# Performance work log

Measured on AMD Instinct MI355X. Metric: run time of the kernel, lower is better.

Reference implementation:

```python
import jax, jax.numpy as jnp
import numpy as np

B, N, D = 131072, 5, 12   # batch, objects per scene, per-object feature dim
E = 64                    # goal embedding / F1 output dim
H = E // 2                # F1 hidden dim = 32


def setup_inputs() -> dict:
    key = jax.random.key(0)
    ks = jax.random.split(key, 6)
    return {
        "obs": jax.random.normal(ks[0], (B, N, D), dtype=jnp.float32),
        "ghat": jax.random.normal(ks[1], (B, E), dtype=jnp.float32),
        "W1": jax.random.normal(ks[2], (2 * D, H), dtype=jnp.float32) * 0.1,
        "b1": jax.random.normal(ks[3], (H,), dtype=jnp.float32) * 0.1,
        "W2": jax.random.normal(ks[4], (H, E), dtype=jnp.float32) * 0.1,
        "b2": jax.random.normal(ks[5], (E,), dtype=jnp.float32) * 0.1,
    }


def reference(obs, ghat, W1, b1, W2, b2):
    b, n, d = obs.shape
    # all-pairs concat: pairs[i,j,k] = cat(obs[i,j], obs[i,k])  -> [B,N,N,2D]
    o_j = jnp.broadcast_to(obs[:, :, None, :], (b, n, n, d))
    o_k = jnp.broadcast_to(obs[:, None, :, :], (b, n, n, d))
    pairs = jnp.concatenate([o_j, o_k], axis=-1)
    # F1 MLP: Linear -> ReLU -> Linear  -> Z [B,N,N,E]
    Z = jnp.maximum(pairs @ W1 + b1, 0.0) @ W2 + b2
    # attention logits w[i,j,k] = <Z[i,j,k], ghat[i]>; softmax over all N*N pairs
    w = jnp.einsum('bjke,be->bjk', Z, ghat)
    p = jax.nn.softmax(w.reshape(b, -1), axis=1).reshape(b, n, n)
    # z_vector[i,j,k] = sum_e p[i,j,k]*Z[i,j,k,e]; zhat[i,j] = sum_k z_vector
    zhat = jnp.einsum('bjk,bjk->bj', p, Z.sum(axis=-1))  # [B,N]
    # state_rep[i,j] = cat(obs[i,j], ghat[i], zhat[i])  -> [B,N,D+E+N]
    state = jnp.concatenate([
        obs,
        jnp.broadcast_to(ghat[:, None, :], (b, n, E)),
        jnp.broadcast_to(zhat[:, None, :], (b, n, n)),
    ], axis=-1)
    return state.reshape(b, -1)  # Flatten -> [B, N*(D+E+N)] = [B, 405]
```

## Files before the change

kernel.cpp:

```cpp
#include <hip/hip_runtime.h>

#define BLOCK 256
#define NB 5
#define DD 12
#define EE 64
#define HH 32
#define ROW 81
#define OUTW 405
#define TILE 64

__global__ __launch_bounds__(BLOCK) void zhat_kernel(
    const float* __restrict__ obs, const float* __restrict__ ghat,
    const float* __restrict__ W1, const float* __restrict__ b1,
    const float* __restrict__ W2, const float* __restrict__ b2,
    float* __restrict__ zbuf, int zstride, int zoff, int B)
{
    __shared__ float s_w2s[HH];
    __shared__ float s_sb2;
    __shared__ float s_g2[BLOCK * 33];

    const int tid = threadIdx.x;

    if (tid < HH) {
        float s = 0.f;
        #pragma unroll
        for (int e = 0; e < EE; ++e) s += W2[tid * EE + e];
        s_w2s[tid] = s;
    } else if (tid == HH) {
        float s = 0.f;
        #pragma unroll
        for (int e = 0; e < EE; ++e) s += b2[e];
        s_sb2 = s;
    }

    const int i = blockIdx.x * BLOCK + tid;

    float g2[HH];
    #pragma unroll
    for (int h = 0; h < HH; ++h) g2[h] = 0.f;
    if (i < B) {
        const float* grow = ghat + (size_t)i * EE;
        #pragma unroll
        for (int e0 = 0; e0 < EE; e0 += 16) {
            float gc[16];
            const float4* gp = reinterpret_cast<const float4*>(grow + e0);
            #pragma unroll
            for (int q = 0; q < 4; ++q) {
                float4 v = gp[q];
                gc[4*q+0] = v.x; gc[4*q+1] = v.y; gc[4*q+2] = v.z; gc[4*q+3] = v.w;
            }
            #pragma unroll
            for (int h = 0; h < HH; ++h) {
                #pragma unroll
                for (int q = 0; q < 16; ++q)
                    g2[h] += W2[h * EE + e0 + q] * gc[q];
            }
        }
    }
    #pragma unroll
    for (int h = 0; h < HH; ++h) s_g2[tid * 33 + h] = g2[h];
    __syncthreads();

    if (i < B) {
        float o[NB * DD];
        {
            const float4* p = reinterpret_cast<const float4*>(obs + (size_t)i * (NB * DD));
            #pragma unroll
            for (int q = 0; q < NB * DD / 4; ++q) {
                float4 v = p[q];
                o[4*q+0] = v.x; o[4*q+1] = v.y; o[4*q+2] = v.z; o[4*q+3] = v.w;
            }
        }

        float w[NB * NB];
        float hw[NB * NB];
        #pragma unroll
        for (int q = 0; q < NB * NB; ++q) { w[q] = 0.f; hw[q] = 0.f; }

        for (int c = 0; c < HH / 8; ++c) {
            float g2c[8], w2c[8];
            #pragma unroll
            for (int hp = 0; hp < 8; ++hp) {
                g2c[hp] = s_g2[tid * 33 + c * 8 + hp];
                w2c[hp] = s_w2s[c * 8 + hp];
            }
            #pragma unroll
            for (int hp = 0; hp < 8; ++hp) {
                const int h = c * 8 + hp;
                float a[NB], bb[NB];
                #pragma unroll
                for (int j = 0; j < NB; ++j) {
                    float acc = b1[h];
                    float accb = 0.f;
                    #pragma unroll
                    for (int d = 0; d < DD; ++d) {
                        acc  += o[j*DD + d] * W1[d*HH + h];
                        accb += o[j*DD + d] * W1[(DD + d)*HH + h];
                    }
                    a[j] = acc; bb[j] = accb;
                }
                #pragma unroll
                for (int j = 0; j < NB; ++j) {
                    #pragma unroll
                    for (int k = 0; k < NB; ++k) {
                        float hv = fmaxf(a[j] + bb[k], 0.f);
                        w[j*NB + k]  += hv * g2c[hp];
                        hw[j*NB + k] += hv * w2c[hp];
                    }
                }
            }
        }

        float m = w[0];
        #pragma unroll
        for (int q = 1; q < NB * NB; ++q) m = fmaxf(m, w[q]);
        float l = 0.f;
        float zacc[NB], racc[NB];
        #pragma unroll
        for (int j = 0; j < NB; ++j) { zacc[j] = 0.f; racc[j] = 0.f; }
        #pragma unroll
        for (int j = 0; j < NB; ++j) {
            #pragma unroll
            for (int k = 0; k < NB; ++k) {
                float e = __expf(w[j*NB + k] - m);
                l += e;
                zacc[j] += e * hw[j*NB + k];
                racc[j] += e;
            }
        }
        const float invl = 1.f / l;
        const float sb2 = s_sb2;
        float* zr = zbuf + (size_t)i * zstride + zoff;
        #pragma unroll
        for (int j = 0; j < NB; ++j)
            zr[j] = (zacc[j] + sb2 * racc[j]) * invl;
    }
}

__global__ __launch_bounds__(BLOCK) void assemble_kernel(
    const float* __restrict__ obs, const float* __restrict__ ghat,
    const float* __restrict__ zbuf, int zstride, int zoff,
    float* __restrict__ out, int B)
{
    __shared__ float s_obs[TILE * NB * DD];
    __shared__ float s_gh[TILE * EE];
    __shared__ float s_zh[TILE * NB];

    const int tid = threadIdx.x;
    const int r0 = blockIdx.x * TILE;
    const int rows = (B - r0 < TILE) ? (B - r0) : TILE;

    for (int t = tid; t < rows * NB * DD; t += BLOCK)
        s_obs[t] = obs[(size_t)r0 * NB * DD + t];
    for (int t = tid; t < rows * EE; t += BLOCK)
        s_gh[t] = ghat[(size_t)r0 * EE + t];
    for (int t = tid; t < rows * NB; t += BLOCK) {
        const int row = t / NB, k = t - row * NB;
        s_zh[t] = zbuf[(size_t)(r0 + row) * zstride + zoff + k];
    }
    __syncthreads();

    const size_t base = (size_t)r0 * OUTW;
    for (int t = tid; t < rows * OUTW; t += BLOCK) {
        const int il = t / OUTW;
        const int r  = t - il * OUTW;
        const int j  = r / ROW;
        const int rr = r - j * ROW;
        float v;
        if (rr < DD)           v = s_obs[il * NB * DD + j * DD + rr];
        else if (rr < DD + EE) v = s_gh[il * EE + (rr - DD)];
        else                   v = s_zh[il * NB + (rr - (DD + EE))];
        out[base + t] = v;
    }
}

extern "C" void kernel_launch(void* const* d_in, const int* in_sizes, int n_in,
                              void* d_out, int out_size, void* d_ws, size_t ws_size,
                              hipStream_t stream) {
    const float* obs  = (const float*)d_in[0];
    const float* ghat = (const float*)d_in[1];
    const float* W1   = (const float*)d_in[2];
    const float* b1   = (const float*)d_in[3];
    const float* W2   = (const float*)d_in[4];
    const float* b2   = (const float*)d_in[5];
    float* out = (float*)d_out;

    const int B = in_sizes[0] / (NB * DD);

    float* zbuf; int zstride, zoff;
    if (ws_size >= (size_t)B * NB * sizeof(float)) {
        zbuf = (float*)d_ws; zstride = NB;   zoff = 0;
    } else {
        zbuf = out;          zstride = OUTW; zoff = OUTW - NB;
    }

    const int gridA = (B + BLOCK - 1) / BLOCK;
    hipLaunchKernelGGL(zhat_kernel, dim3(gridA), dim3(BLOCK), 0, stream,
                       obs, ghat, W1, b1, W2, b2, zbuf, zstride, zoff, B);

    const int gridB = (B + TILE - 1) / TILE;
    hipLaunchKernelGGL(assemble_kernel, dim3(gridB), dim3(BLOCK), 0, stream,
                       obs, ghat, zbuf, zstride, zoff, out, B);
}
```

Measured before the change: 146.5 us.

## Map one scene per 32-lane group with shared-memory staging and shuffle softmax

Restructures zhat_kernel so each block handles 8 scenes and each 32-lane group handles one scene. Lanes split the hidden units when computing the per-object W1 projections and the ghat·W2 products, then split the 25 pairs for the logits, with the softmax done through cross-lane shuffles. This replaces the one-thread-per-scene design, which carried large per-thread register arrays and a big shared buffer, and it removes the redundant per-thread W1 and W2 work. In exchange there are many more blocks, two extra barriers, and per-block reloads of the weights.

```diff
diff --git a/kernel.cpp b/kernel.cpp
--- a/kernel.cpp
+++ b/kernel.cpp
@@ -8,6 +8,9 @@
 #define ROW 81
 #define OUTW 405
 #define TILE 64
+#define S8 8
+#define ABS 36
+#define G2S 36
 
 __global__ __launch_bounds__(BLOCK) void zhat_kernel(
     const float* __restrict__ obs, const float* __restrict__ ghat,
@@ -15,126 +18,122 @@
     const float* __restrict__ W2, const float* __restrict__ b2,
     float* __restrict__ zbuf, int zstride, int zoff, int B)
 {
+    __shared__ float s_obs[S8 * 60];
+    __shared__ float s_gh[S8 * EE];
+    __shared__ float s_ab[S8 * 10 * ABS];
+    __shared__ float s_g2[S8 * G2S];
     __shared__ float s_w2s[HH];
     __shared__ float s_sb2;
-    __shared__ float s_g2[BLOCK * 33];
-
-    const int tid = threadIdx.x;
-
-    if (tid < HH) {
+
+    const int tid  = threadIdx.x;
+    const int h    = tid & 31;
+    const int sb   = tid >> 5;
+    const int blk0 = blockIdx.x * S8;
+
+    for (int idx = tid; idx < S8 * 60; idx += BLOCK) {
+        const int sc = idx / 60, dd = idx - sc * 60;
+        int gi = blk0 + sc; if (gi >= B) gi = B - 1;
+        s_obs[idx] = obs[(size_t)gi * 60 + dd];
+    }
+    for (int idx = tid; idx < S8 * EE; idx += BLOCK) {
+        const int sc = idx >> 6, e = idx & 63;
+        int gi = blk0 + sc; if (gi >= B) gi = B - 1;
+        s_gh[idx] = ghat[(size_t)gi * EE + e];
+    }
+    if (tid == 0) {
         float s = 0.f;
+        const float4* p = reinterpret_cast<const float4*>(b2);
         #pragma unroll
-        for (int e = 0; e < EE; ++e) s += W2[tid * EE + e];
-        s_w2s[tid] = s;
-    } else if (tid == HH) {
-        float s = 0.f;
+        for (int q = 0; q < EE / 4; ++q) { float4 v = p[q]; s += (v.x + v.y) + (v.z + v.w); }
+        s_sb2 = s;
+    }
+    __syncthreads();
+
+    {
+        float w1c[24];
         #pragma unroll
-        for (int e = 0; e < EE; ++e) s += b2[e];
-        s_sb2 = s;
-    }
-
-    const int i = blockIdx.x * BLOCK + tid;
-
-    float g2[HH];
+        for (int dd = 0; dd < 24; ++dd) w1c[dd] = W1[dd * HH + h];
+        const float b1h = b1[h];
+        #pragma unroll 2
+        for (int q = 0; q < 10; ++q) {
+            const int rs    = sb + S8 * q;
+            const int scene = rs / 10;
+            const int row   = rs - scene * 10;
+            const int jr    = (row < 5) ? row : row - 5;
+            const float* op = &s_obs[scene * 60 + jr * DD];
+            float accA = b1h, accB = 0.f;
+            #pragma unroll
+            for (int c = 0; c < 3; ++c) {
+                const float4 o4 = *reinterpret_cast<const float4*>(op + 4 * c);
+                accA += (o4.x * w1c[4*c+0] + o4.y * w1c[4*c+1])
+                      + (o4.z * w1c[4*c+2] + o4.w * w1c[4*c+3]);
+                accB += (o4.x * w1c[12+4*c+0] + o4.y * w1c[12+4*c+1])
+                      + (o4.z * w1c[12+4*c+2] + o4.w * w1c[12+4*c+3]);
+            }
+            s_ab[(scene * 10 + row) * ABS + h] = (row < 5) ? accA : accB;
+        }
+    }
+
+    {
+        const float4* w2r = reinterpret_cast<const float4*>(W2 + h * EE);
+        const float4* ghr = reinterpret_cast<const float4*>(&s_gh[sb * EE]);
+        float g2 = 0.f, ws = 0.f;
+        #pragma unroll
+        for (int ec = 0; ec < EE / 4; ++ec) {
+            const float4 wv = w2r[ec];
+            const float4 gv = ghr[ec];
+            g2 += (wv.x * gv.x + wv.y * gv.y) + (wv.z * gv.z + wv.w * gv.w);
+            ws += (wv.x + wv.y) + (wv.z + wv.w);
+        }
+        s_g2[sb * G2S + h] = g2;
+        if (sb == 0) s_w2s[h] = ws;
+    }
+    __syncthreads();
+
+    const int j5 = h / 5, k5 = h - j5 * 5;
+    const float* arow = &s_ab[(sb * 10 + j5) * ABS];
+    const float* brow = &s_ab[(sb * 10 + 5 + k5) * ABS];
+    const float* g2p  = &s_g2[sb * G2S];
+    float wp = (h < 25) ? 0.f : -1e30f;
+    float hp = 0.f;
     #pragma unroll
-    for (int h = 0; h < HH; ++h) g2[h] = 0.f;
-    if (i < B) {
-        const float* grow = ghat + (size_t)i * EE;
-        #pragma unroll
-        for (int e0 = 0; e0 < EE; e0 += 16) {
-            float gc[16];
-            const float4* gp = reinterpret_cast<const float4*>(grow + e0);
-            #pragma unroll
-            for (int q = 0; q < 4; ++q) {
-                float4 v = gp[q];
-                gc[4*q+0] = v.x; gc[4*q+1] = v.y; gc[4*q+2] = v.z; gc[4*q+3] = v.w;
-            }
-            #pragma unroll
-            for (int h = 0; h < HH; ++h) {
-                #pragma unroll
-                for (int q = 0; q < 16; ++q)
-                    g2[h] += W2[h * EE + e0 + q] * gc[q];
-            }
-        }
-    }
+    for (int h4 = 0; h4 < 8; ++h4) {
+        const float4 a4 = *reinterpret_cast<const float4*>(arow + 4 * h4);
+        const float4 b4 = *reinterpret_cast<const float4*>(brow + 4 * h4);
+        const float4 g4 = *reinterpret_cast<const float4*>(g2p + 4 * h4);
+        const float4 w4 = *reinterpret_cast<const float4*>(&s_w2s[4 * h4]);
+        float hv;
+        hv = fmaxf(a4.x + b4.x, 0.f); wp += hv * g4.x; hp += hv * w4.x;
+        hv = fmaxf(a4.y + b4.y, 0.f); wp += hv * g4.y; hp += hv * w4.y;
+        hv = fmaxf(a4.z + b4.z, 0.f); wp += hv * g4.z; hp += hv * w4.z;
+        hv = fmaxf(a4.w + b4.w, 0.f); wp += hv * g4.w; hp += hv * w4.w;
+    }
+
+    float m = wp;
+    m = fmaxf(m, __shfl_xor(m, 1));
+    m = fmaxf(m, __shfl_xor(m, 2));
+    m = fmaxf(m, __shfl_xor(m, 4));
+    m = fmaxf(m, __shfl_xor(m, 8));
+    m = fmaxf(m, __shfl_xor(m, 16));
+    const float e = __expf(wp - m);
+    float l = e;
+    l += __shfl_xor(l, 1);
+    l += __shfl_xor(l, 2);
+    l += __shfl_xor(l, 4);
+    l += __shfl_xor(l, 8);
+    l += __shfl_xor(l, 16);
+    const float c = e * (hp + s_sb2);
+
+    const int lane  = tid & 63;
+    const int sbase = lane & 32;
+    const int jj    = (h < 5) ? h : 0;
+    float z = 0.f;
     #pragma unroll
-    for (int h = 0; h < HH; ++h) s_g2[tid * 33 + h] = g2[h];
-    __syncthreads();
-
-    if (i < B) {
-        float o[NB * DD];
-        {
-            const float4* p = reinterpret_cast<const float4*>(obs + (size_t)i * (NB * DD));
-            #pragma unroll
-            for (int q = 0; q < NB * DD / 4; ++q) {
-                float4 v = p[q];
-                o[4*q+0] = v.x; o[4*q+1] = v.y; o[4*q+2] = v.z; o[4*q+3] = v.w;
-            }
-        }
-
-        float w[NB * NB];
-        float hw[NB * NB];
-        #pragma unroll
-        for (int q = 0; q < NB * NB; ++q) { w[q] = 0.f; hw[q] = 0.f; }
-
-        for (int c = 0; c < HH / 8; ++c) {
-            float g2c[8], w2c[8];
-            #pragma unroll
-            for (int hp = 0; hp < 8; ++hp) {
-                g2c[hp] = s_g2[tid * 33 + c * 8 + hp];
-                w2c[hp] = s_w2s[c * 8 + hp];
-            }
-            #pragma unroll
-            for (int hp = 0; hp < 8; ++hp) {
-                const int h = c * 8 + hp;
-                float a[NB], bb[NB];
-                #pragma unroll
-                for (int j = 0; j < NB; ++j) {
-                    float acc = b1[h];
-                    float accb = 0.f;
-                    #pragma unroll
-                    for (int d = 0; d < DD; ++d) {
-                        acc  += o[j*DD + d] * W1[d*HH + h];
-                        accb += o[j*DD + d] * W1[(DD + d)*HH + h];
-                    }
-                    a[j] = acc; bb[j] = accb;
-                }
-                #pragma unroll
-                for (int j = 0; j < NB; ++j) {
-                    #pragma unroll
-                    for (int k = 0; k < NB; ++k) {
-                        float hv = fmaxf(a[j] + bb[k], 0.f);
-                        w[j*NB + k]  += hv * g2c[hp];
-                        hw[j*NB + k] += hv * w2c[hp];
-                    }
-                }
-            }
-        }
-
-        float m = w[0];
-        #pragma unroll
-        for (int q = 1; q < NB * NB; ++q) m = fmaxf(m, w[q]);
-        float l = 0.f;
-        float zacc[NB], racc[NB];
-        #pragma unroll
-        for (int j = 0; j < NB; ++j) { zacc[j] = 0.f; racc[j] = 0.f; }
-        #pragma unroll
-        for (int j = 0; j < NB; ++j) {
-            #pragma unroll
-            for (int k = 0; k < NB; ++k) {
-                float e = __expf(w[j*NB + k] - m);
-                l += e;
-                zacc[j] += e * hw[j*NB + k];
-                racc[j] += e;
-            }
-        }
-        const float invl = 1.f / l;
-        const float sb2 = s_sb2;
-        float* zr = zbuf + (size_t)i * zstride + zoff;
-        #pragma unroll
-        for (int j = 0; j < NB; ++j)
-            zr[j] = (zacc[j] + sb2 * racc[j]) * invl;
-    }
+    for (int k = 0; k < 5; ++k)
+        z += __shfl(c, sbase + jj * 5 + k);
+    const int isc = blk0 + sb;
+    if (h < 5 && isc < B)
+        zbuf[(size_t)isc * zstride + zoff + h] = z / l;
 }
 
 __global__ __launch_bounds__(BLOCK) void assemble_kernel(
@@ -194,7 +193,7 @@
         zbuf = out;          zstride = OUTW; zoff = OUTW - NB;
     }
 
-    const int gridA = (B + BLOCK - 1) / BLOCK;
+    const int gridA = (B + S8 - 1) / S8;
     hipLaunchKernelGGL(zhat_kernel, dim3(gridA), dim3(BLOCK), 0, stream,
                        obs, ghat, W1, b1, W2, b2, zbuf, zstride, zoff, B);
 
```

Measured after the change: 235.7 us. 60.9% more time.
